# Optimization experiments

Measured on AMD Instinct MI355X. Metric: run time of the kernel, lower is better.

The kernel has to match this reference:

```python
import jax, jax.numpy as jnp
import numpy as np

N, D, K = 10240, 256, 30  # nodes, feature dim, top-k
EPS = 1e-12  # F.normalize eps


def setup_inputs() -> dict:
    key = jax.random.key(0)
    k1, _ = jax.random.split(key)
    features = jax.random.normal(k1, (N, D), dtype=jnp.float32)
    # Attentive layers: elementwise feature weights, initialized to ones (as in the repo)
    w1 = jnp.ones((D,), dtype=jnp.float32)
    w2 = jnp.ones((D,), dtype=jnp.float32)
    return {"features": features, "w1": w1, "w2": w2, "k": K}


def reference(features, w1, w2, k):
    # internal_forward: Attentive = x * w (x @ diag(w)); relu between layers (mlp_act='relu')
    h = jax.nn.relu(features * w1) * w2              # [N, D]
    # F.normalize(dim=1, p=2) with eps clamp
    norm = jnp.maximum(jnp.linalg.norm(h, axis=1, keepdims=True), EPS)
    emb = h / norm                                   # [N, D]
    # cal_similarity_graph: dense cosine similarity
    sim = emb @ emb.T                                # [N, N]
    # top_k(sim, k+1): keep top (k+1) entries per row, zero the rest
    _, idx = jax.lax.top_k(sim, k + 1)               # [N, k+1]
    rows = jnp.arange(sim.shape[0])[:, None]
    mask = jnp.zeros_like(sim).at[rows, idx].set(1.0)
    # apply_non_linearity with 'relu'
    return jax.nn.relu(sim * mask)
```

## Files before the change

kernel.cpp:

```cpp
#include <hip/hip_runtime.h>
#include <math.h>

#define N_NODES 10240
#define DIM 256
#define TPB 256
#define CAP 1536

typedef _Float16 half8 __attribute__((ext_vector_type(8)));
typedef float f32x4 __attribute__((ext_vector_type(4)));

__device__ __forceinline__ void async_load16(const void* g, void* l) {
  __builtin_amdgcn_global_load_lds(
      (const __attribute__((address_space(1))) unsigned int*)g,
      (__attribute__((address_space(3))) unsigned int*)l, 16, 0, 0);
}

__global__ __launch_bounds__(256) void norm_split_kernel(
    const float* __restrict__ F, const float* __restrict__ w1,
    const float* __restrict__ w2, _Float16* __restrict__ P0,
    _Float16* __restrict__ P1) {
  int row = blockIdx.x, tid = threadIdx.x;
  __shared__ float red[TPB];
  size_t base = (size_t)row * DIM + tid;
  float h = fmaxf(F[base] * w1[tid], 0.0f) * w2[tid];
  red[tid] = h * h;
  __syncthreads();
  for (int o = TPB / 2; o > 0; o >>= 1) {
    if (tid < o) red[tid] += red[tid + o];
    __syncthreads();
  }
  float e = h / fmaxf(sqrtf(red[0]), 1e-12f);
  _Float16 p0 = (_Float16)e;
  _Float16 p1 = (_Float16)((e - (float)p0) * 2048.0f);
  P0[base] = p0;
  P1[base] = p1;
}

__global__ __launch_bounds__(256) void gemm_mfma_kernel(
    const _Float16* __restrict__ P0, const _Float16* __restrict__ P1,
    float* __restrict__ C) {
  __shared__ char smem[32768];
  char* AsB = smem;
  char* BsB = smem + 16384;

  int tid = threadIdx.x;
  int lane = tid & 63;
  int w = tid >> 6;
  int wr = (w >> 1) * 64;
  int wc = (w & 1) * 64;
  int quad = lane >> 4;
  int mr = lane & 15;
  int rowBase = blockIdx.y * 128;
  int colBase = blockIdx.x * 128;

  size_t rowOffA[4], rowOffB[4];
  int ldsOff[4];
#pragma unroll
  for (int i = 0; i < 4; ++i) {
    int u = tid + i * 256;
    int m = u >> 3;
    int g = (u & 7) ^ (m & 7);
    ldsOff[i] = u * 16;
    rowOffA[i] = (size_t)(rowBase + m) * DIM + g * 8;
    rowOffB[i] = (size_t)(colBase + m) * DIM + g * 8;
  }

  int fOffA[2][4], fOffB[2][4];
#pragma unroll
  for (int s = 0; s < 2; ++s)
#pragma unroll
    for (int t = 0; t < 4; ++t) {
      int g = s * 4 + quad;
      int mA = wr + t * 16 + mr;
      fOffA[s][t] = (mA * 8 + (g ^ (mA & 7))) * 16;
      int mB = wc + t * 16 + mr;
      fOffB[s][t] = (mB * 8 + (g ^ (mB & 7))) * 16;
    }

  f32x4 acc[4][4];
#pragma unroll
  for (int t = 0; t < 4; ++t)
#pragma unroll
    for (int u2 = 0; u2 < 4; ++u2) acc[t][u2] = (f32x4)0.0f;

  const _Float16* Aseg[3] = {P0, P1, P0};
  const _Float16* Bseg[3] = {P1, P0, P0};

  for (int pass = 0; pass < 3; ++pass) {
    if (pass == 2) {
      const float sc = 1.0f / 2048.0f;
#pragma unroll
      for (int t = 0; t < 4; ++t)
#pragma unroll
        for (int u2 = 0; u2 < 4; ++u2)
#pragma unroll
          for (int r = 0; r < 4; ++r) acc[t][u2][r] *= sc;
    }
    const _Float16* Ap = Aseg[pass];
    const _Float16* Bp = Bseg[pass];
    for (int c = 0; c < 4; ++c) {
      int kb = c * 64;
#pragma unroll
      for (int i = 0; i < 4; ++i)
        async_load16(Ap + rowOffA[i] + kb, AsB + ldsOff[i]);
#pragma unroll
      for (int i = 0; i < 4; ++i)
        async_load16(Bp + rowOffB[i] + kb, BsB + ldsOff[i]);
      __syncthreads();
#pragma unroll
      for (int s = 0; s < 2; ++s) {
        half8 af[4], bf[4];
#pragma unroll
        for (int t = 0; t < 4; ++t) {
          af[t] = *(const half8*)(AsB + fOffA[s][t]);
          bf[t] = *(const half8*)(BsB + fOffB[s][t]);
        }
#pragma unroll
        for (int t = 0; t < 4; ++t)
#pragma unroll
          for (int u2 = 0; u2 < 4; ++u2)
            acc[t][u2] = __builtin_amdgcn_mfma_f32_16x16x32_f16(
                af[t], bf[u2], acc[t][u2], 0, 0, 0);
      }
      __syncthreads();
    }
  }

#pragma unroll
  for (int t = 0; t < 4; ++t) {
    int gr = rowBase + wr + t * 16 + quad * 4;
#pragma unroll
    for (int u2 = 0; u2 < 4; ++u2) {
      int gc = colBase + wc + u2 * 16 + mr;
      float* cp = C + (size_t)gr * N_NODES + gc;
      cp[0] = acc[t][u2][0];
      cp[(size_t)N_NODES] = acc[t][u2][1];
      cp[(size_t)2 * N_NODES] = acc[t][u2][2];
      cp[(size_t)3 * N_NODES] = acc[t][u2][3];
    }
  }
}

__global__ __launch_bounds__(256) void topk_kernel(
    float* __restrict__ C, const int* __restrict__ kptr) {
  constexpr int EPT = N_NODES / TPB;
  constexpr int NV4 = EPT / 4;
  __shared__ unsigned int lm[TPB];
  __shared__ unsigned int cu[CAP];
  __shared__ int ci[CAP];
  __shared__ unsigned int s_cnt, s_L31, s_Tu;
  __shared__ int s_Jcut;

  int tid = threadIdx.x;
  float* Crow = C + (size_t)blockIdx.x * N_NODES;
  unsigned int want = (unsigned int)(kptr[0] + 1);

  unsigned int u[EPT];
  unsigned int lmax = 0u;
#pragma unroll
  for (int i = 0; i < NV4; ++i) {
    float4 v = *(const float4*)&Crow[(i * TPB + tid) * 4];
    float fv[4] = {v.x, v.y, v.z, v.w};
#pragma unroll
    for (int c = 0; c < 4; ++c) {
      unsigned int s = __float_as_uint(fv[c]);
      unsigned int m = (s & 0x80000000u) ? ~s : (s | 0x80000000u);
      u[i * 4 + c] = m;
      lmax = (m > lmax) ? m : lmax;
    }
  }
  lm[tid] = lmax;
  if (tid == 0) s_cnt = 0u;
  __syncthreads();

  {
    unsigned int r = 0;
    for (int j = 0; j < TPB; ++j) {
      unsigned int vj = lm[j];
      r += (vj > lmax) || (vj == lmax && j < tid);
    }
    if (r == want - 1) s_L31 = lmax;
  }
  __syncthreads();
  unsigned int L31 = s_L31;

#pragma unroll
  for (int i = 0; i < EPT; ++i) {
    if (u[i] >= L31) {
      unsigned int pos = atomicAdd(&s_cnt, 1u);
      if (pos < CAP) {
        cu[pos] = u[i];
        ci[pos] = ((i / 4) * TPB + tid) * 4 + (i % 4);
      }
    }
  }
  __syncthreads();
  unsigned int c_total = s_cnt;

  if (c_total <= CAP) {
    for (unsigned int i = tid; i < c_total; i += TPB) {
      unsigned int ui = cu[i];
      int ii = ci[i];
      unsigned int r = 0;
      for (unsigned int j = 0; j < c_total; ++j) {
        unsigned int uj = cu[j];
        r += (uj > ui) || (uj == ui && ci[j] < ii);
      }
      if (r == want - 1) { s_Tu = ui; s_Jcut = ii; }
    }
    __syncthreads();
  } else {
    unsigned int lo = 0u, hi = 0xFFFFFFFFu;
    while (lo < hi) {
      unsigned int mid = lo + ((hi - lo) >> 1);
      unsigned int cnt = 0;
#pragma unroll
      for (int i = 0; i < EPT; ++i) cnt += (u[i] > mid) ? 1u : 0u;
      lm[tid] = cnt;
      __syncthreads();
      for (int o = TPB / 2; o > 0; o >>= 1) {
        if (tid < o) lm[tid] += lm[tid + o];
        __syncthreads();
      }
      unsigned int gcnt = lm[0];
      __syncthreads();
      if (gcnt < want) hi = mid; else lo = mid + 1u;
    }
    unsigned int Tu = lo;
    unsigned int cnt = 0;
#pragma unroll
    for (int i = 0; i < EPT; ++i) cnt += (u[i] > Tu) ? 1u : 0u;
    lm[tid] = cnt;
    __syncthreads();
    for (int o = TPB / 2; o > 0; o >>= 1) {
      if (tid < o) lm[tid] += lm[tid + o];
      __syncthreads();
    }
    unsigned int need = want - lm[0];
    __syncthreads();
    int jlo = 0, jhi = N_NODES - 1;
    while (jlo < jhi) {
      int jmid = (jlo + jhi) >> 1;
      unsigned int cc = 0;
#pragma unroll
      for (int i = 0; i < EPT; ++i) {
        int jj = ((i / 4) * TPB + tid) * 4 + (i % 4);
        cc += (u[i] == Tu && jj <= jmid) ? 1u : 0u;
      }
      lm[tid] = cc;
      __syncthreads();
      for (int o = TPB / 2; o > 0; o >>= 1) {
        if (tid < o) lm[tid] += lm[tid + o];
        __syncthreads();
      }
      unsigned int tot = lm[0];
      __syncthreads();
      if (tot >= need) jhi = jmid; else jlo = jmid + 1;
    }
    if (tid == 0) { s_Tu = Tu; s_Jcut = jlo; }
    __syncthreads();
  }

  unsigned int Tu = s_Tu;
  int Jcut = s_Jcut;

#pragma unroll
  for (int i = 0; i < NV4; ++i) {
    float out[4];
#pragma unroll
    for (int c = 0; c < 4; ++c) {
      unsigned int m = u[i * 4 + c];
      int j = (i * TPB + tid) * 4 + c;
      bool keep = (m > Tu) || (m == Tu && j <= Jcut);
      float v = __uint_as_float((m & 0x80000000u) ? (m ^ 0x80000000u) : ~m);
      out[c] = (keep && v > 0.0f) ? v : 0.0f;
    }
    *(float4*)&Crow[(i * TPB + tid) * 4] =
        make_float4(out[0], out[1], out[2], out[3]);
  }
}

extern "C" void kernel_launch(void* const* d_in, const int* in_sizes, int n_in,
                              void* d_out, int out_size, void* d_ws, size_t ws_size,
                              hipStream_t stream) {
  const float* F  = (const float*)d_in[0];
  const float* w1 = (const float*)d_in[1];
  const float* w2 = (const float*)d_in[2];
  const int*   kp = (const int*)d_in[3];
  float* C = (float*)d_out;
  _Float16* P0 = (_Float16*)d_ws;
  _Float16* P1 = P0 + (size_t)N_NODES * DIM;

  norm_split_kernel<<<N_NODES, DIM, 0, stream>>>(F, w1, w2, P0, P1);

  dim3 grid(N_NODES / 128, N_NODES / 128);
  gemm_mfma_kernel<<<grid, 256, 0, stream>>>(P0, P1, C);

  topk_kernel<<<N_NODES, TPB, 0, stream>>>(C, kp);
}
```

Before: 668.1 us.

## Exploit similarity symmetry: compute upper-triangle GEMM tiles and mirror-write them

The 2D GEMM grid becomes a 1D grid over upper-triangular 128x128 tile pairs. Each block recovers its (by, bx) tile coordinates with a closed-form square root plus correction loops. Off-diagonal tiles also write their transposed result into the mirror location, which roughly halves the MFMA work and the operand loads. In exchange, the mirrored stores are 16-byte vectors scattered across many rows, so they coalesce poorly, and the total output write volume stays the same.

After: 674.7 us. Within noise of the previous version (+1.0%).

```diff
diff --git a/kernel.cpp b/kernel.cpp
--- a/kernel.cpp
+++ b/kernel.cpp
@@ -5,6 +5,8 @@
 #define DIM 256
 #define TPB 256
 #define CAP 1536
+#define NB (N_NODES / 128)
+#define NTRI (NB * (NB + 1) / 2)
 
 typedef _Float16 half8 __attribute__((ext_vector_type(8)));
 typedef float f32x4 __attribute__((ext_vector_type(4)));
@@ -50,8 +52,21 @@
   int wc = (w & 1) * 64;
   int quad = lane >> 4;
   int mr = lane & 15;
-  int rowBase = blockIdx.y * 128;
-  int colBase = blockIdx.x * 128;
+
+  int t0 = blockIdx.x;
+  int by;
+  {
+    float a = 2.0f * NB + 1.0f;
+    float disc = a * a - 8.0f * (float)t0;
+    by = (int)((a - sqrtf(disc)) * 0.5f);
+    if (by > NB - 1) by = NB - 1;
+    if (by < 0) by = 0;
+    while (by > 0 && by * NB - (by * (by - 1)) / 2 > t0) --by;
+    while (by < NB - 1 && (by + 1) * NB - ((by + 1) * by) / 2 <= t0) ++by;
+  }
+  int bx = by + (t0 - (by * NB - (by * (by - 1)) / 2));
+  int rowBase = by * 128;
+  int colBase = bx * 128;
 
   size_t rowOffA[4], rowOffB[4];
   int ldsOff[4];
@@ -137,6 +152,17 @@
       cp[(size_t)N_NODES] = acc[t][u2][1];
       cp[(size_t)2 * N_NODES] = acc[t][u2][2];
       cp[(size_t)3 * N_NODES] = acc[t][u2][3];
+    }
+  }
+  if (bx != by) {
+#pragma unroll
+    for (int t = 0; t < 4; ++t) {
+      int gr = rowBase + wr + t * 16 + quad * 4;
+#pragma unroll
+      for (int u2 = 0; u2 < 4; ++u2) {
+        int gc = colBase + wc + u2 * 16 + mr;
+        *(f32x4*)(C + (size_t)gc * N_NODES + gr) = acc[t][u2];
+      }
     }
   }
 }
@@ -293,8 +319,7 @@
 
   norm_split_kernel<<<N_NODES, DIM, 0, stream>>>(F, w1, w2, P0, P1);
 
-  dim3 grid(N_NODES / 128, N_NODES / 128);
-  gemm_mfma_kernel<<<grid, 256, 0, stream>>>(P0, P1, C);
+  gemm_mfma_kernel<<<NTRI, 256, 0, stream>>>(P0, P1, C);
 
   topk_kernel<<<N_NODES, TPB, 0, stream>>>(C, kp);
 }
```

## Exploit symmetry of similarity matrix: compute upper-triangle tiles and mirror-store

Applied to the files above, without the earlier changes.

Launches only the upper-triangular set of 128x128 tiles of emb·embᵀ and writes each off-diagonal tile both directly and transposed, roughly halving the MFMA work. It also simplifies address math by using 32-bit byte offsets and an XOR for the k-subslice, and sets a launch-bounds occupancy hint of 4. The mirrored store writes float4 columns with a large stride, so it is poorly coalesced and adds write traffic cost. The three-pass split result is not bitwise symmetric, but the two mirrored halves differ only by rounding.

New measurement: 778.8 us. +16.6%, slower.

```diff
diff --git a/kernel.cpp b/kernel.cpp
--- a/kernel.cpp
+++ b/kernel.cpp
@@ -5,6 +5,8 @@
 #define DIM 256
 #define TPB 256
 #define CAP 1536
+#define NB (N_NODES / 128)
+#define NTRI (NB * (NB + 1) / 2)
 
 typedef _Float16 half8 __attribute__((ext_vector_type(8)));
 typedef float f32x4 __attribute__((ext_vector_type(4)));
@@ -36,7 +38,7 @@
   P1[base] = p1;
 }
 
-__global__ __launch_bounds__(256) void gemm_mfma_kernel(
+__global__ __launch_bounds__(256, 4) void gemm_mfma_kernel(
     const _Float16* __restrict__ P0, const _Float16* __restrict__ P1,
     float* __restrict__ C) {
   __shared__ char smem[32768];
@@ -50,32 +52,32 @@
   int wc = (w & 1) * 64;
   int quad = lane >> 4;
   int mr = lane & 15;
-  int rowBase = blockIdx.y * 128;
-  int colBase = blockIdx.x * 128;
-
-  size_t rowOffA[4], rowOffB[4];
-  int ldsOff[4];
+
+  int by = 0, rem = blockIdx.x;
+  while (rem >= NB - by) { rem -= NB - by; ++by; }
+  int bx = by + rem;
+  int rowBase = by * 128;
+  int colBase = bx * 128;
+
+  int gOffA[4], gOffB[4], ldsOff[4];
 #pragma unroll
   for (int i = 0; i < 4; ++i) {
     int u = tid + i * 256;
     int m = u >> 3;
     int g = (u & 7) ^ (m & 7);
     ldsOff[i] = u * 16;
-    rowOffA[i] = (size_t)(rowBase + m) * DIM + g * 8;
-    rowOffB[i] = (size_t)(colBase + m) * DIM + g * 8;
-  }
-
-  int fOffA[2][4], fOffB[2][4];
-#pragma unroll
-  for (int s = 0; s < 2; ++s)
-#pragma unroll
-    for (int t = 0; t < 4; ++t) {
-      int g = s * 4 + quad;
-      int mA = wr + t * 16 + mr;
-      fOffA[s][t] = (mA * 8 + (g ^ (mA & 7))) * 16;
-      int mB = wc + t * 16 + mr;
-      fOffB[s][t] = (mB * 8 + (g ^ (mB & 7))) * 16;
-    }
+    gOffA[i] = ((rowBase + m) * DIM + g * 8) * 2;
+    gOffB[i] = ((colBase + m) * DIM + g * 8) * 2;
+  }
+
+  int fA[4], fB[4];
+#pragma unroll
+  for (int t = 0; t < 4; ++t) {
+    int mA = wr + t * 16 + mr;
+    fA[t] = (mA * 8 + (quad ^ (mA & 7))) * 16;
+    int mB = wc + t * 16 + mr;
+    fB[t] = (mB * 8 + (quad ^ (mB & 7))) * 16;
+  }
 
   f32x4 acc[4][4];
 #pragma unroll
@@ -96,24 +98,25 @@
 #pragma unroll
           for (int r = 0; r < 4; ++r) acc[t][u2][r] *= sc;
     }
-    const _Float16* Ap = Aseg[pass];
-    const _Float16* Bp = Bseg[pass];
+    const char* Ap = (const char*)Aseg[pass];
+    const char* Bp = (const char*)Bseg[pass];
     for (int c = 0; c < 4; ++c) {
-      int kb = c * 64;
+      int kb = c * 128;
 #pragma unroll
       for (int i = 0; i < 4; ++i)
-        async_load16(Ap + rowOffA[i] + kb, AsB + ldsOff[i]);
+        async_load16(Ap + gOffA[i] + kb, AsB + ldsOff[i]);
 #pragma unroll
       for (int i = 0; i < 4; ++i)
-        async_load16(Bp + rowOffB[i] + kb, BsB + ldsOff[i]);
+        async_load16(Bp + gOffB[i] + kb, BsB + ldsOff[i]);
       __syncthreads();
 #pragma unroll
       for (int s = 0; s < 2; ++s) {
+        int sx = s * 64;
         half8 af[4], bf[4];
 #pragma unroll
         for (int t = 0; t < 4; ++t) {
-          af[t] = *(const half8*)(AsB + fOffA[s][t]);
-          bf[t] = *(const half8*)(BsB + fOffB[s][t]);
+          af[t] = *(const half8*)(AsB + (fA[t] ^ sx));
+          bf[t] = *(const half8*)(BsB + (fB[t] ^ sx));
         }
 #pragma unroll
         for (int t = 0; t < 4; ++t)
@@ -126,6 +129,7 @@
     }
   }
 
+  bool mirror = (bx != by);
 #pragma unroll
   for (int t = 0; t < 4; ++t) {
     int gr = rowBase + wr + t * 16 + quad * 4;
@@ -137,6 +141,8 @@
       cp[(size_t)N_NODES] = acc[t][u2][1];
       cp[(size_t)2 * N_NODES] = acc[t][u2][2];
       cp[(size_t)3 * N_NODES] = acc[t][u2][3];
+      if (mirror)
+        *(f32x4*)(C + (size_t)gc * N_NODES + gr) = acc[t][u2];
     }
   }
 }
@@ -293,8 +299,7 @@
 
   norm_split_kernel<<<N_NODES, DIM, 0, stream>>>(F, w1, w2, P0, P1);
 
-  dim3 grid(N_NODES / 128, N_NODES / 128);
-  gemm_mfma_kernel<<<grid, 256, 0, stream>>>(P0, P1, C);
+  gemm_mfma_kernel<<<NTRI, 256, 0, stream>>>(P0, P1, C);
 
   topk_kernel<<<N_NODES, TPB, 0, stream>>>(C, kp);
 }
```

## Emit per-chunk row maxima from GEMM to prune top-k candidate scan

Applied to the files above, without the earlier changes.

The GEMM epilogue now writes the max of each 64-column chunk per row into a workspace summary. A new top-k kernel uses those maxima to pick a threshold from the k+1-th largest chunk max and scans only the qualifying chunks for candidates. It then zero-fills the row and scatters the survivors, instead of reading the full 40 KB row into registers. This adds a shuffle reduction and extra global stores to the GEMM, and it depends on the workspace being large enough, otherwise it falls back to the old kernel.

New measurement: 745.6 us. +11.6%, slower.

```diff
diff --git a/kernel.cpp b/kernel.cpp
--- a/kernel.cpp
+++ b/kernel.cpp
@@ -5,6 +5,9 @@
 #define DIM 256
 #define TPB 256
 #define CAP 1536
+#define CAP2 2048
+#define NCH 160
+#define CHW 64
 
 typedef _Float16 half8 __attribute__((ext_vector_type(8)));
 typedef float f32x4 __attribute__((ext_vector_type(4)));
@@ -13,6 +16,14 @@
   __builtin_amdgcn_global_load_lds(
       (const __attribute__((address_space(1))) unsigned int*)g,
       (__attribute__((address_space(3))) unsigned int*)l, 16, 0, 0);
+}
+
+__device__ __forceinline__ unsigned int fmap(float f) {
+  unsigned int s = __float_as_uint(f);
+  return (s & 0x80000000u) ? ~s : (s | 0x80000000u);
+}
+__device__ __forceinline__ float funmap(unsigned int m) {
+  return __uint_as_float((m & 0x80000000u) ? (m ^ 0x80000000u) : ~m);
 }
 
 __global__ __launch_bounds__(256) void norm_split_kernel(
@@ -38,7 +49,7 @@
 
 __global__ __launch_bounds__(256) void gemm_mfma_kernel(
     const _Float16* __restrict__ P0, const _Float16* __restrict__ P1,
-    float* __restrict__ C) {
+    float* __restrict__ C, float* __restrict__ S) {
   __shared__ char smem[32768];
   char* AsB = smem;
   char* BsB = smem + 16384;
@@ -139,6 +150,177 @@
       cp[(size_t)3 * N_NODES] = acc[t][u2][3];
     }
   }
+
+  if (S != nullptr) {
+    int chunk = blockIdx.x * 2 + (w & 1);
+#pragma unroll
+    for (int t = 0; t < 4; ++t)
+#pragma unroll
+      for (int r = 0; r < 4; ++r) {
+        float m4 = fmaxf(fmaxf(acc[t][0][r], acc[t][1][r]),
+                         fmaxf(acc[t][2][r], acc[t][3][r]));
+        m4 = fmaxf(m4, __shfl_xor(m4, 1, 64));
+        m4 = fmaxf(m4, __shfl_xor(m4, 2, 64));
+        m4 = fmaxf(m4, __shfl_xor(m4, 4, 64));
+        m4 = fmaxf(m4, __shfl_xor(m4, 8, 64));
+        if (mr == 0) {
+          int gr = rowBase + wr + t * 16 + quad * 4 + r;
+          S[(size_t)gr * NCH + chunk] = m4;
+        }
+      }
+  }
+}
+
+__global__ __launch_bounds__(256) void topk_sum_kernel(
+    float* __restrict__ C, const float* __restrict__ S,
+    const int* __restrict__ kptr) {
+  constexpr int EPT = N_NODES / TPB;
+  constexpr int NV4 = EPT / 4;
+  __shared__ unsigned int sm[NCH];
+  __shared__ unsigned short qlist[NCH];
+  __shared__ unsigned int cu[CAP2];
+  __shared__ int ci[CAP2];
+  __shared__ unsigned int lm[TPB];
+  __shared__ unsigned int s_cnt, s_q, s_Tpre, s_Tu;
+  __shared__ int s_Jcut;
+
+  int tid = threadIdx.x;
+  float* Crow = C + (size_t)blockIdx.x * N_NODES;
+  const float* Srow = S + (size_t)blockIdx.x * NCH;
+  unsigned int want = (unsigned int)(kptr[0] + 1);
+
+  if (tid == 0) { s_cnt = 0u; s_q = 0u; s_Tpre = 0u; }
+  if (tid < NCH) sm[tid] = fmap(Srow[tid]);
+  __syncthreads();
+
+  if (tid < NCH && want <= NCH) {
+    unsigned int mv = sm[tid];
+    unsigned int r = 0;
+    for (int j = 0; j < NCH; ++j) {
+      unsigned int vj = sm[j];
+      r += (vj > mv) || (vj == mv && j < tid);
+    }
+    if (r == want - 1) s_Tpre = mv;
+  }
+  __syncthreads();
+  unsigned int Tp = s_Tpre;
+
+  if (tid < NCH && sm[tid] >= Tp) qlist[atomicAdd(&s_q, 1u)] = (unsigned short)tid;
+  __syncthreads();
+  unsigned int nq = s_q;
+
+  for (unsigned int idx = tid; idx < nq * CHW; idx += TPB) {
+    int c = qlist[idx >> 6];
+    int col = c * CHW + (int)(idx & 63u);
+    unsigned int m = fmap(Crow[col]);
+    if (m >= Tp) {
+      unsigned int p = atomicAdd(&s_cnt, 1u);
+      if (p < CAP2) { cu[p] = m; ci[p] = col; }
+    }
+  }
+  __syncthreads();
+  unsigned int ct = s_cnt;
+
+  if (ct <= CAP2) {
+    for (unsigned int i = tid; i < ct; i += TPB) {
+      unsigned int ui = cu[i];
+      int ii = ci[i];
+      unsigned int r = 0;
+      for (unsigned int j = 0; j < ct; ++j) {
+        unsigned int uj = cu[j];
+        r += (uj > ui) || (uj == ui && ci[j] < ii);
+      }
+      if (r == want - 1) { s_Tu = ui; s_Jcut = ii; }
+    }
+    __syncthreads();
+    unsigned int Tu = s_Tu;
+    int Jcut = s_Jcut;
+
+#pragma unroll
+    for (int i = 0; i < NV4; ++i)
+      *(float4*)&Crow[(i * TPB + tid) * 4] = make_float4(0.f, 0.f, 0.f, 0.f);
+    __syncthreads();
+    for (unsigned int i = tid; i < ct; i += TPB) {
+      unsigned int m = cu[i];
+      int col = ci[i];
+      if ((m > Tu) || (m == Tu && col <= Jcut)) {
+        float v = funmap(m);
+        if (v > 0.0f) Crow[col] = v;
+      }
+    }
+  } else {
+    unsigned int u[EPT];
+#pragma unroll
+    for (int i = 0; i < NV4; ++i) {
+      float4 v = *(const float4*)&Crow[(i * TPB + tid) * 4];
+      float fv[4] = {v.x, v.y, v.z, v.w};
+#pragma unroll
+      for (int c = 0; c < 4; ++c) u[i * 4 + c] = fmap(fv[c]);
+    }
+    unsigned int lo = 0u, hi = 0xFFFFFFFFu;
+    while (lo < hi) {
+      unsigned int mid = lo + ((hi - lo) >> 1);
+      unsigned int cnt = 0;
+#pragma unroll
+      for (int i = 0; i < EPT; ++i) cnt += (u[i] > mid) ? 1u : 0u;
+      lm[tid] = cnt;
+      __syncthreads();
+      for (int o = TPB / 2; o > 0; o >>= 1) {
+        if (tid < o) lm[tid] += lm[tid + o];
+        __syncthreads();
+      }
+      unsigned int gcnt = lm[0];
+      __syncthreads();
+      if (gcnt < want) hi = mid; else lo = mid + 1u;
+    }
+    unsigned int Tu = lo;
+    unsigned int cnt = 0;
+#pragma unroll
+    for (int i = 0; i < EPT; ++i) cnt += (u[i] > Tu) ? 1u : 0u;
+    lm[tid] = cnt;
+    __syncthreads();
+    for (int o = TPB / 2; o > 0; o >>= 1) {
+      if (tid < o) lm[tid] += lm[tid + o];
+      __syncthreads();
+    }
+    unsigned int need = want - lm[0];
+    __syncthreads();
+    int jlo = 0, jhi = N_NODES - 1;
+    while (jlo < jhi) {
+      int jmid = (jlo + jhi) >> 1;
+      unsigned int cc = 0;
+#pragma unroll
+      for (int i = 0; i < EPT; ++i) {
+        int jj = ((i / 4) * TPB + tid) * 4 + (i % 4);
+        cc += (u[i] == Tu && jj <= jmid) ? 1u : 0u;
+      }
+      lm[tid] = cc;
+      __syncthreads();
+      for (int o = TPB / 2; o > 0; o >>= 1) {
+        if (tid < o) lm[tid] += lm[tid + o];
+        __syncthreads();
+      }
+      unsigned int tot = lm[0];
+      __syncthreads();
+      if (tot >= need) jhi = jmid; else jlo = jmid + 1;
+    }
+    unsigned int TuF = Tu;
+    int JcF = jlo;
+#pragma unroll
+    for (int i = 0; i < NV4; ++i) {
+      float out[4];
+#pragma unroll
+      for (int c = 0; c < 4; ++c) {
+        unsigned int m = u[i * 4 + c];
+        int j = (i * TPB + tid) * 4 + c;
+        bool keep = (m > TuF) || (m == TuF && j <= JcF);
+        float v = funmap(m);
+        out[c] = (keep && v > 0.0f) ? v : 0.0f;
+      }
+      *(float4*)&Crow[(i * TPB + tid) * 4] =
+          make_float4(out[0], out[1], out[2], out[3]);
+    }
+  }
 }
 
 __global__ __launch_bounds__(256) void topk_kernel(
@@ -163,8 +345,7 @@
     float fv[4] = {v.x, v.y, v.z, v.w};
 #pragma unroll
     for (int c = 0; c < 4; ++c) {
-      unsigned int s = __float_as_uint(fv[c]);
-      unsigned int m = (s & 0x80000000u) ? ~s : (s | 0x80000000u);
+      unsigned int m = fmap(fv[c]);
       u[i * 4 + c] = m;
       lmax = (m > lmax) ? m : lmax;
     }
@@ -272,7 +453,7 @@
       unsigned int m = u[i * 4 + c];
       int j = (i * TPB + tid) * 4 + c;
       bool keep = (m > Tu) || (m == Tu && j <= Jcut);
-      float v = __uint_as_float((m & 0x80000000u) ? (m ^ 0x80000000u) : ~m);
+      float v = funmap(m);
       out[c] = (keep && v > 0.0f) ? v : 0.0f;
     }
     *(float4*)&Crow[(i * TPB + tid) * 4] =
@@ -291,10 +472,17 @@
   _Float16* P0 = (_Float16*)d_ws;
   _Float16* P1 = P0 + (size_t)N_NODES * DIM;
 
+  size_t pbytes = (size_t)N_NODES * DIM * sizeof(_Float16);
+  size_t need = 2 * pbytes + (size_t)N_NODES * NCH * sizeof(float);
+  float* S = (ws_size >= need) ? (float*)((char*)d_ws + 2 * pbytes) : nullptr;
+
   norm_split_kernel<<<N_NODES, DIM, 0, stream>>>(F, w1, w2, P0, P1);
 
   dim3 grid(N_NODES / 128, N_NODES / 128);
-  gemm_mfma_kernel<<<grid, 256, 0, stream>>>(P0, P1, C);
-
-  topk_kernel<<<N_NODES, TPB, 0, stream>>>(C, kp);
-}
+  gemm_mfma_kernel<<<grid, 256, 0, stream>>>(P0, P1, C, S);
+
+  if (S != nullptr)
+    topk_sum_kernel<<<N_NODES, TPB, 0, stream>>>(C, S, kp);
+  else
+    topk_kernel<<<N_NODES, TPB, 0, stream>>>(C, kp);
+}
```
